# Performance work log

Measured on AMD Instinct MI355X. Metric: run time of the kernel, lower is better.

## Reference

```python
import jax, jax.numpy as jnp
import numpy as np

B, H, W, DIM, HEADS, WS, SHIFT, MLP_RATIO = 32, 56, 56, 256, 8, 7, 3, 4
N = WS * WS                      # tokens per window = 49
NW = (H // WS) * (W // WS)       # windows per image = 64
HEAD_DIM = DIM // HEADS
HIDDEN = DIM * MLP_RATIO


def _rel_index():
    # standard Swin relative position index, shape (N, N), values in [0, (2*WS-1)^2)
    coords = np.stack(np.meshgrid(np.arange(WS), np.arange(WS), indexing='ij')).reshape(2, -1)
    rel = (coords[:, :, None] - coords[:, None, :]).transpose(1, 2, 0)
    rel[:, :, 0] += WS - 1
    rel[:, :, 1] += WS - 1
    rel[:, :, 0] *= 2 * WS - 1
    return rel.sum(-1).astype(np.int32)


def _attn_mask():
    # shifted-window attention mask, shape (NW, N, N), values in {0, -100}
    img = np.zeros((H, W))
    slices = (slice(0, -WS), slice(-WS, -SHIFT), slice(-SHIFT, None))
    cnt = 0
    for hs in slices:
        for ws_ in slices:
            img[hs, ws_] = cnt
            cnt += 1
    mw = img.reshape(H // WS, WS, W // WS, WS).transpose(0, 2, 1, 3).reshape(-1, N)
    diff = mw[:, None, :] - mw[:, :, None]
    return np.where(diff != 0, -100.0, 0.0).astype(np.float32)


def setup_inputs() -> dict:
    key = jax.random.key(0)
    ks = jax.random.split(key, 16)
    s = 0.02
    return {
        'x': jax.random.normal(ks[0], (B, H * W, DIM), jnp.float32),
        'norm1_w': jnp.ones((DIM,), jnp.float32),
        'norm1_b': jnp.zeros((DIM,), jnp.float32),
        'qkv_w': jax.random.normal(ks[1], (3 * DIM, DIM), jnp.float32) * s,
        'qkv_b': jnp.zeros((3 * DIM,), jnp.float32),
        'rpb_table': jax.random.normal(ks[2], ((2 * WS - 1) ** 2, HEADS), jnp.float32) * s,
        'proj_w': jax.random.normal(ks[3], (DIM, DIM), jnp.float32) * s,
        'proj_b': jnp.zeros((DIM,), jnp.float32),
        'norm2_w': jnp.ones((DIM,), jnp.float32),
        'norm2_b': jnp.zeros((DIM,), jnp.float32),
        'fc1_w': jax.random.normal(ks[4], (HIDDEN, DIM), jnp.float32) * s,
        'fc1_b': jnp.zeros((HIDDEN,), jnp.float32),
        'fc2_w': jax.random.normal(ks[5], (DIM, HIDDEN), jnp.float32) * s,
        'fc2_b': jnp.zeros((DIM,), jnp.float32),
        'rel_idx': jnp.asarray(_rel_index()),
        'attn_mask': jnp.asarray(_attn_mask()),
    }


def _ln(t, w, b):
    mu = t.mean(-1, keepdims=True)
    var = ((t - mu) ** 2).mean(-1, keepdims=True)
    return (t - mu) * jax.lax.rsqrt(var + 1e-5) * w + b


def reference(x, norm1_w, norm1_b, qkv_w, qkv_b, rpb_table, proj_w, proj_b,
              norm2_w, norm2_b, fc1_w, fc1_b, fc2_w, fc2_b, rel_idx, attn_mask):
    Bz = x.shape[0]
    shortcut = x
    h = _ln(x, norm1_w, norm1_b).reshape(Bz, H, W, DIM)
    h = jnp.roll(h, (-SHIFT, -SHIFT), axis=(1, 2))                      # cyclic shift
    # window partition -> (Bz*NW, N, C)
    h = h.reshape(Bz, H // WS, WS, W // WS, WS, DIM).transpose(0, 1, 3, 2, 4, 5).reshape(-1, N, DIM)
    qkv = (h @ qkv_w.T + qkv_b).reshape(-1, N, 3, HEADS, HEAD_DIM).transpose(2, 0, 3, 1, 4)
    q, k, v = qkv[0], qkv[1], qkv[2]                                    # (Bz*NW, heads, N, d)
    scale = HEAD_DIM ** -0.5
    attn = jnp.einsum('whnd,whmd->whnm', q * scale, k)
    bias = rpb_table[rel_idx].transpose(2, 0, 1)                        # (heads, N, N)
    attn = attn + bias[None]
    attn = attn.reshape(Bz, NW, HEADS, N, N) + attn_mask[None, :, None]  # shift mask
    attn = jax.nn.softmax(attn.reshape(-1, HEADS, N, N), axis=-1)
    out = jnp.einsum('whnm,whmd->whnd', attn, v).transpose(0, 2, 1, 3).reshape(-1, N, DIM)
    out = out @ proj_w.T + proj_b
    # window reverse + un-shift
    out = out.reshape(Bz, H // WS, W // WS, WS, WS, DIM).transpose(0, 1, 3, 2, 4, 5).reshape(Bz, H, W, DIM)
    out = jnp.roll(out, (SHIFT, SHIFT), axis=(1, 2)).reshape(Bz, H * W, DIM)
    x = shortcut + out
    # residual MLP (pre-LN), exact GELU as in nn.GELU default
    h2 = _ln(x, norm2_w, norm2_b)
    h2 = jax.nn.gelu(h2 @ fc1_w.T + fc1_b, approximate=False)
    return x + (h2 @ fc2_w.T + fc2_b)
```

## Files before the change

kernel.cpp:

```cpp
#include <hip/hip_runtime.h>

typedef unsigned short ushort_t;
typedef __attribute__((ext_vector_type(8))) __bf16 bf16x8;
typedef __attribute__((ext_vector_type(4))) float floatx4;

#define TOKS 100352

__device__ __forceinline__ ushort_t f2bf(float f) {
    union { float f; unsigned u; } a; a.f = f;
    unsigned r = a.u + 0x7fffu + ((a.u >> 16) & 1u);
    return (ushort_t)(r >> 16);
}

__device__ __forceinline__ void async16(const void* g, void* l) {
    __builtin_amdgcn_global_load_lds(
        (const __attribute__((address_space(1))) unsigned int*)g,
        (__attribute__((address_space(3))) unsigned int*)l,
        16, 0, 0);
}

__device__ __forceinline__ int win_to_orig(int t) {
    int b = t / 3136, rr = t - b * 3136;
    int w_ = rr / 49, pos = rr - w_ * 49;
    int wi = w_ >> 3, wj = w_ & 7;
    int ti = pos / 7, tj = pos - ti * 7;
    int h = wi * 7 + ti + 3; if (h >= 56) h -= 56;
    int w = wj * 7 + tj + 3; if (w >= 56) w -= 56;
    return b * 3136 + h * 56 + w;
}

__global__ void convert_kernel(const float* __restrict__ qkv_w, const float* __restrict__ proj_w,
                               const float* __restrict__ fc1_w, const float* __restrict__ fc2_w,
                               const float* __restrict__ rpb, const int* __restrict__ rel_idx,
                               ushort_t* __restrict__ wq, ushort_t* __restrict__ wp,
                               ushort_t* __restrict__ w1, ushort_t* __restrict__ w2,
                               float* __restrict__ bias_h) {
    int i = blockIdx.x * 256 + threadIdx.x;
    if (i < 196608) wq[i] = f2bf(qkv_w[i]);
    if (i < 65536)  wp[i] = f2bf(proj_w[i]);
    if (i < 262144) { w1[i] = f2bf(fc1_w[i]); w2[i] = f2bf(fc2_w[i]); }
    if (i < 19208) {
        int h = i / 2401, ij = i - h * 2401;
        bias_h[i] = rpb[rel_idx[ij] * 8 + h];
    }
}

__global__ __launch_bounds__(256) void ln_kernel(const float* __restrict__ xin,
                                                 const float* __restrict__ gw,
                                                 const float* __restrict__ gb,
                                                 ushort_t* __restrict__ outb) {
    const int wid = threadIdx.x >> 6, lane = threadIdx.x & 63;
    const int t_out = blockIdx.x * 4 + wid;
    const int t_in = win_to_orig(t_out);
    const float4* src = (const float4*)(xin + (long)t_in * 256);
    float4 v = src[lane];
    float s  = v.x + v.y + v.z + v.w;
    float s2 = v.x*v.x + v.y*v.y + v.z*v.z + v.w*v.w;
    #pragma unroll
    for (int d = 32; d >= 1; d >>= 1) { s += __shfl_xor(s, d, 64); s2 += __shfl_xor(s2, d, 64); }
    float mu  = s * 0.00390625f;
    float var = s2 * 0.00390625f - mu * mu;
    float ry  = rsqrtf(var + 1e-5f);
    float4 w4 = ((const float4*)gw)[lane], b4 = ((const float4*)gb)[lane];
    unsigned long long p =
          (unsigned long long)f2bf((v.x - mu) * ry * w4.x + b4.x)
        | ((unsigned long long)f2bf((v.y - mu) * ry * w4.y + b4.y) << 16)
        | ((unsigned long long)f2bf((v.z - mu) * ry * w4.z + b4.z) << 32)
        | ((unsigned long long)f2bf((v.w - mu) * ry * w4.w + b4.w) << 48);
    ((unsigned long long*)(outb + (long)t_out * 256))[lane] = p;
}

template <int MODE, int N_LD, int KD>
__global__ __launch_bounds__(256, 2) void gemm_kernel(const ushort_t* __restrict__ A,
                                                      const ushort_t* __restrict__ Bw,
                                                      const float* __restrict__ bias,
                                                      void* __restrict__ outp,
                                                      const ushort_t* __restrict__ x1w,
                                                      int rowOff) {
    __shared__ __align__(16) ushort_t As[128 * 32];
    __shared__ __align__(16) ushort_t Bs[128 * 32];
    const int tid = threadIdx.x;
    const int lane = tid & 63;
    const int wid = tid >> 6;
    const int wm = wid & 1, wn = wid >> 1;
    const int l15 = lane & 15, quad = lane >> 4;
    const long tileM = (long)blockIdx.y * 128;
    const long tileN = (long)blockIdx.x * 128;

    floatx4 acc[4][4];
    #pragma unroll
    for (int i = 0; i < 4; i++)
        #pragma unroll
        for (int j = 0; j < 4; j++) acc[i][j] = {0.f, 0.f, 0.f, 0.f};

    const int o1 = tid * 16;
    const int r1 = o1 >> 6, c1 = (o1 & 63) >> 1;
    const ushort_t* Ar1 = A + (tileM + r1) * KD + c1;
    const ushort_t* Ar2 = A + (tileM + r1 + 64) * KD + c1;
    const ushort_t* Br1 = Bw + (tileN + r1) * KD + c1;
    const ushort_t* Br2 = Bw + (tileN + r1 + 64) * KD + c1;
    ushort_t* Ad1 = &As[o1 >> 1];
    ushort_t* Ad2 = &As[(o1 >> 1) + 2048];
    ushort_t* Bd1 = &Bs[o1 >> 1];
    ushort_t* Bd2 = &Bs[(o1 >> 1) + 2048];

    for (int k0 = 0; k0 < KD; k0 += 32) {
        async16(Ar1 + k0, Ad1);
        async16(Ar2 + k0, Ad2);
        async16(Br1 + k0, Bd1);
        async16(Br2 + k0, Bd2);
        __syncthreads();
        bf16x8 af[4], bfr[4];
        #pragma unroll
        for (int mi = 0; mi < 4; mi++)
            af[mi] = *(const bf16x8*)&As[(wm * 64 + mi * 16 + l15) * 32 + quad * 8];
        #pragma unroll
        for (int nj = 0; nj < 4; nj++)
            bfr[nj] = *(const bf16x8*)&Bs[(wn * 64 + nj * 16 + l15) * 32 + quad * 8];
        #pragma unroll
        for (int mi = 0; mi < 4; mi++)
            #pragma unroll
            for (int nj = 0; nj < 4; nj++)
                acc[mi][nj] = __builtin_amdgcn_mfma_f32_16x16x32_bf16(af[mi], bfr[nj], acc[mi][nj], 0, 0, 0);
        __syncthreads();
    }

    #pragma unroll
    for (int mi = 0; mi < 4; mi++)
      #pragma unroll
      for (int nj = 0; nj < 4; nj++)
        #pragma unroll
        for (int r = 0; r < 4; r++) {
            long row = tileM + wm * 64 + mi * 16 + quad * 4 + r;
            long col = tileN + wn * 64 + nj * 16 + l15;
            float v = acc[mi][nj][r] + bias[col];
            if (MODE == 0) {
                ((ushort_t*)outp)[row * N_LD + col] = f2bf(v);
            } else if (MODE == 2) {
                float g = 0.5f * v * (1.f + erff(v * 0.70710678118654752f));
                ((ushort_t*)outp)[row * N_LD + col] = f2bf(g);
            } else {
                union { ushort_t u[2]; unsigned v32; float f; } cvt;
                cvt.u[0] = 0; cvt.u[1] = x1w[row * 256 + col];
                float res = cvt.f;
                int orig = win_to_orig((int)row + rowOff);
                ((float*)outp)[(long)orig * 256 + col] = v + res;
            }
        }
}

__global__ __launch_bounds__(256, 2) void proj_ln_kernel(
        const ushort_t* __restrict__ A, const ushort_t* __restrict__ Bw,
        const float* __restrict__ pb, const float* __restrict__ x_res,
        const float* __restrict__ n2w, const float* __restrict__ n2b,
        ushort_t* __restrict__ x1w, ushort_t* __restrict__ h2out) {
    __shared__ __align__(16) ushort_t As[64 * 32];
    __shared__ __align__(16) ushort_t Bs[256 * 32];
    __shared__ float red_s[4][64];
    __shared__ float red_q[4][64];
    const int tid = threadIdx.x, lane = tid & 63, wid = tid >> 6;
    const int l15 = lane & 15, quad = lane >> 4;
    const long tileM = (long)blockIdx.x * 64;

    floatx4 acc[4][4];
    #pragma unroll
    for (int i = 0; i < 4; i++)
        #pragma unroll
        for (int j = 0; j < 4; j++) acc[i][j] = {0.f, 0.f, 0.f, 0.f};

    const int oA = tid * 16;
    const int rA = oA >> 6, cA = (oA & 63) >> 1;
    const ushort_t* Ap = A + (tileM + rA) * 256 + cA;
    ushort_t* Ad = &As[oA >> 1];

    for (int k0 = 0; k0 < 256; k0 += 32) {
        async16(Ap + k0, Ad);
        #pragma unroll
        for (int ch = 0; ch < 4; ch++) {
            int o = ch * 4096 + oA;
            async16(Bw + (o >> 6) * 256 + ((o & 63) >> 1) + k0, &Bs[o >> 1]);
        }
        __syncthreads();
        bf16x8 af[4], bfr[4];
        #pragma unroll
        for (int mi = 0; mi < 4; mi++)
            af[mi] = *(const bf16x8*)&As[(mi * 16 + l15) * 32 + quad * 8];
        #pragma unroll
        for (int nj = 0; nj < 4; nj++)
            bfr[nj] = *(const bf16x8*)&Bs[(wid * 64 + nj * 16 + l15) * 32 + quad * 8];
        #pragma unroll
        for (int mi = 0; mi < 4; mi++)
            #pragma unroll
            for (int nj = 0; nj < 4; nj++)
                acc[mi][nj] = __builtin_amdgcn_mfma_f32_16x16x32_bf16(af[mi], bfr[nj], acc[mi][nj], 0, 0, 0);
        __syncthreads();
    }

    #pragma unroll
    for (int mi = 0; mi < 4; mi++)
      #pragma unroll
      for (int r = 0; r < 4; r++) {
        int iloc = mi * 16 + quad * 4 + r;
        int orig = win_to_orig((int)tileM + iloc);
        float s = 0.f, q = 0.f;
        #pragma unroll
        for (int nj = 0; nj < 4; nj++) {
            int col = wid * 64 + nj * 16 + l15;
            float v = acc[mi][nj][r] + pb[col] + x_res[(long)orig * 256 + col];
            x1w[(tileM + iloc) * 256 + col] = f2bf(v);
            acc[mi][nj][r] = v;
            s += v; q += v * v;
        }
        #pragma unroll
        for (int d = 1; d < 16; d <<= 1) { s += __shfl_xor(s, d, 64); q += __shfl_xor(q, d, 64); }
        if (l15 == 0) { red_s[wid][iloc] = s; red_q[wid][iloc] = q; }
      }
    __syncthreads();
    #pragma unroll
    for (int mi = 0; mi < 4; mi++)
      #pragma unroll
      for (int r = 0; r < 4; r++) {
        int iloc = mi * 16 + quad * 4 + r;
        float s = red_s[0][iloc] + red_s[1][iloc] + red_s[2][iloc] + red_s[3][iloc];
        float q = red_q[0][iloc] + red_q[1][iloc] + red_q[2][iloc] + red_q[3][iloc];
        float mu = s * 0.00390625f;
        float var = q * 0.00390625f - mu * mu;
        float rstd = rsqrtf(var + 1e-5f);
        #pragma unroll
        for (int nj = 0; nj < 4; nj++) {
            int col = wid * 64 + nj * 16 + l15;
            float v = acc[mi][nj][r];
            h2out[(tileM + iloc) * 256 + col] = f2bf((v - mu) * rstd * n2w[col] + n2b[col]);
        }
      }
}

__global__ __launch_bounds__(128) void attn_kernel(const ushort_t* __restrict__ qkv,
                                                   const float* __restrict__ bias_h,
                                                   const float* __restrict__ mask,
                                                   ushort_t* __restrict__ attnout) {
    __shared__ __align__(16) ushort_t lds[2 * 6912];
    const int tid = threadIdx.x, lane = tid & 63, wid = tid >> 6;
    ushort_t* Pl = &lds[wid * 6912];
    ushort_t* Vt = Pl + 64 * 72;
    const int whid = blockIdx.x * 2 + wid;
    const int win = whid >> 3, head = whid & 7;
    const int l15 = lane & 15, quad = lane >> 4;
    const long base = (long)win * 49 * 768;
    const float* bh = bias_h + head * 2401;
    const float* mk = mask + (win & 63) * 2401;

    bf16x8 qf[4], kf[4];
    #pragma unroll
    for (int t4 = 0; t4 < 4; t4++) {
        int tok = t4 * 16 + l15; if (tok > 48) tok = 48;
        const ushort_t* p = qkv + base + (long)tok * 768 + head * 32 + quad * 8;
        qf[t4] = *(const bf16x8*)p;
        kf[t4] = *(const bf16x8*)(p + 256);
    }

    floatx4 S[4][4];
    #pragma unroll
    for (int mi = 0; mi < 4; mi++)
        #pragma unroll
        for (int nj = 0; nj < 4; nj++) {
            floatx4 z = {0.f, 0.f, 0.f, 0.f};
            S[mi][nj] = __builtin_amdgcn_mfma_f32_16x16x32_bf16(qf[mi], kf[nj], z, 0, 0, 0);
        }

    {
        int j = lane;
        int jc = j < 49 ? j : 48;
        const uint4* vsrc = (const uint4*)(qkv + base + (long)jc * 768 + 512 + head * 32);
        uint4 vz; vz.x = vz.y = vz.z = vz.w = 0u;
        #pragma unroll
        for (int q4 = 0; q4 < 4; q4++) {
            uint4 vv = (j < 49) ? vsrc[q4] : vz;
            int db = q4 * 8;
            Vt[(db+0)*72 + j] = (ushort_t)vv.x;  Vt[(db+1)*72 + j] = (ushort_t)(vv.x >> 16);
            Vt[(db+2)*72 + j] = (ushort_t)vv.y;  Vt[(db+3)*72 + j] = (ushort_t)(vv.y >> 16);
            Vt[(db+4)*72 + j] = (ushort_t)vv.z;  Vt[(db+5)*72 + j] = (ushort_t)(vv.z >> 16);
            Vt[(db+6)*72 + j] = (ushort_t)vv.w;  Vt[(db+7)*72 + j] = (ushort_t)(vv.w >> 16);
        }
    }

    const float scale = 0.17677669529663687f;
    #pragma unroll
    for (int mi = 0; mi < 4; mi++)
      #pragma unroll
      for (int nj = 0; nj < 4; nj++)
        #pragma unroll
        for (int r = 0; r < 4; r++) {
            int i = mi * 16 + quad * 4 + r;
            int j = nj * 16 + l15;
            float s = -1e30f;
            if (i < 49 && j < 49) {
                int ij = i * 49 + j;
                s = S[mi][nj][r] * scale + bh[ij] + mk[ij];
            }
            S[mi][nj][r] = s;
        }

    float rinv[4][4];
    #pragma unroll
    for (int mi = 0; mi < 4; mi++)
      #pragma unroll
      for (int r = 0; r < 4; r++) {
          float m = fmaxf(fmaxf(S[mi][0][r], S[mi][1][r]), fmaxf(S[mi][2][r], S[mi][3][r]));
          #pragma unroll
          for (int d = 1; d < 16; d <<= 1) m = fmaxf(m, __shfl_xor(m, d, 64));
          float e[4], sum = 0.f;
          #pragma unroll
          for (int nj = 0; nj < 4; nj++) { e[nj] = __expf(S[mi][nj][r] - m); sum += e[nj]; }
          #pragma unroll
          for (int d = 1; d < 16; d <<= 1) sum += __shfl_xor(sum, d, 64);
          rinv[mi][r] = 1.f / sum;
          int i = mi * 16 + quad * 4 + r;
          #pragma unroll
          for (int nj = 0; nj < 4; nj++) Pl[i * 72 + (nj * 16 + l15)] = f2bf(e[nj]);
      }

    __syncthreads();

    floatx4 O[4][2];
    #pragma unroll
    for (int mi = 0; mi < 4; mi++) { O[mi][0] = {0.f,0.f,0.f,0.f}; O[mi][1] = {0.f,0.f,0.f,0.f}; }
    #pragma unroll
    for (int kc = 0; kc < 2; kc++) {
        bf16x8 pf[4], vf[2];
        #pragma unroll
        for (int mi = 0; mi < 4; mi++)
            pf[mi] = *(const bf16x8*)&Pl[(mi * 16 + l15) * 72 + kc * 32 + quad * 8];
        #pragma unroll
        for (int n2 = 0; n2 < 2; n2++)
            vf[n2] = *(const bf16x8*)&Vt[(n2 * 16 + l15) * 72 + kc * 32 + quad * 8];
        #pragma unroll
        for (int mi = 0; mi < 4; mi++)
            #pragma unroll
            for (int n2 = 0; n2 < 2; n2++)
                O[mi][n2] = __builtin_amdgcn_mfma_f32_16x16x32_bf16(pf[mi], vf[n2], O[mi][n2], 0, 0, 0);
    }

    #pragma unroll
    for (int mi = 0; mi < 4; mi++)
      #pragma unroll
      for (int n2 = 0; n2 < 2; n2++)
        #pragma unroll
        for (int r = 0; r < 4; r++) {
            int i = mi * 16 + quad * 4 + r;
            if (i < 49) {
                long orow = ((long)win * 49 + i) * 256 + head * 32 + n2 * 16 + l15;
                attnout[orow] = f2bf(O[mi][n2][r] * rinv[mi][r]);
            }
        }
}

extern "C" void kernel_launch(void* const* d_in, const int* in_sizes, int n_in,
                              void* d_out, int out_size, void* d_ws, size_t ws_size,
                              hipStream_t stream) {
    const float* x      = (const float*)d_in[0];
    const float* n1w    = (const float*)d_in[1];
    const float* n1b    = (const float*)d_in[2];
    const float* qkv_w  = (const float*)d_in[3];
    const float* qkv_b  = (const float*)d_in[4];
    const float* rpb    = (const float*)d_in[5];
    const float* proj_w = (const float*)d_in[6];
    const float* proj_b = (const float*)d_in[7];
    const float* n2w    = (const float*)d_in[8];
    const float* n2b    = (const float*)d_in[9];
    const float* fc1_w  = (const float*)d_in[10];
    const float* fc1_b  = (const float*)d_in[11];
    const float* fc2_w  = (const float*)d_in[12];
    const float* fc2_b  = (const float*)d_in[13];
    const int*   rel_idx= (const int*)d_in[14];
    const float* amask  = (const float*)d_in[15];

    char* ws = (char*)d_ws;
    ushort_t* wq   = (ushort_t*)(ws + 0);
    ushort_t* wp   = (ushort_t*)(ws + 393216);
    ushort_t* w1   = (ushort_t*)(ws + 524288);
    ushort_t* w2   = (ushort_t*)(ws + 1048576);
    float*    bh   = (float*)   (ws + 1572864);
    ushort_t* hwin = (ushort_t*)(ws + 1649728);
    ushort_t* qkvb = (ushort_t*)(ws + 53029952);
    ushort_t* h2   = (ushort_t*)(ws + 104410176);
    ushort_t* x1w  = (ushort_t*)(ws + 155790400);
    ushort_t* h3   = hwin;

    convert_kernel<<<1024, 256, 0, stream>>>(qkv_w, proj_w, fc1_w, fc2_w, rpb, rel_idx,
                                             wq, wp, w1, w2, bh);
    ln_kernel<<<TOKS / 4, 256, 0, stream>>>(x, n1w, n1b, hwin);
    gemm_kernel<0, 768, 256><<<dim3(6, 784), 256, 0, stream>>>(hwin, wq, qkv_b, qkvb, nullptr, 0);
    attn_kernel<<<8192, 128, 0, stream>>>(qkvb, bh, amask, hwin);
    proj_ln_kernel<<<1568, 256, 0, stream>>>(hwin, wp, proj_b, x, n2w, n2b, x1w, h2);
    for (int c = 0; c < 2; c++) {
        gemm_kernel<2, 1024, 256><<<dim3(8, 392), 256, 0, stream>>>(
            h2 + (long)c * 50176 * 256, w1, fc1_b, h3, nullptr, 0);
        gemm_kernel<4, 256, 1024><<<dim3(2, 392), 256, 0, stream>>>(
            h3, w2, fc2_b, (float*)d_out, x1w + (long)c * 50176 * 256, c * 50176);
    }
    (void)in_sizes; (void)n_in; (void)out_size; (void)ws_size;
}
```

Before: 750.7 us.

## Premerge bias+mask into bf16 table, swizzle GEMM tiles, widen attention blocks

Precomputes a per-window-per-head bf16 table that combines the relative position bias and the shift mask, stored temporarily in the output buffer. The attention kernel then does one load per score instead of two fp32 loads. GEMM launches switch to a 1D grid that groups tiles so 8 row tiles sweep the column tiles together, aiming for better L2 reuse. Attention blocks now run 4 waves with smaller LDS per wave. The risks are bf16 rounding of bias+mask and relying on the output buffer being overwritten later.

New measurement: 658.7 us. -12.3%, faster.

```diff
diff --git a/kernel.cpp b/kernel.cpp
--- a/kernel.cpp
+++ b/kernel.cpp
@@ -10,6 +10,9 @@
     union { float f; unsigned u; } a; a.f = f;
     unsigned r = a.u + 0x7fffu + ((a.u >> 16) & 1u);
     return (ushort_t)(r >> 16);
+}
+__device__ __forceinline__ float bf2f(ushort_t u) {
+    union { unsigned v; float f; } a; a.v = ((unsigned)u) << 16; return a.f;
 }
 
 __device__ __forceinline__ void async16(const void* g, void* l) {
@@ -32,16 +35,18 @@
 __global__ void convert_kernel(const float* __restrict__ qkv_w, const float* __restrict__ proj_w,
                                const float* __restrict__ fc1_w, const float* __restrict__ fc2_w,
                                const float* __restrict__ rpb, const int* __restrict__ rel_idx,
+                               const float* __restrict__ amask,
                                ushort_t* __restrict__ wq, ushort_t* __restrict__ wp,
                                ushort_t* __restrict__ w1, ushort_t* __restrict__ w2,
-                               float* __restrict__ bias_h) {
+                               ushort_t* __restrict__ bm) {
     int i = blockIdx.x * 256 + threadIdx.x;
     if (i < 196608) wq[i] = f2bf(qkv_w[i]);
     if (i < 65536)  wp[i] = f2bf(proj_w[i]);
     if (i < 262144) { w1[i] = f2bf(fc1_w[i]); w2[i] = f2bf(fc2_w[i]); }
-    if (i < 19208) {
-        int h = i / 2401, ij = i - h * 2401;
-        bias_h[i] = rpb[rel_idx[ij] * 8 + h];
+    if (i < 1229312) {
+        int wh = i / 2401, ij = i - wh * 2401;
+        int head = wh & 7, wimg = wh >> 3;
+        bm[i] = f2bf(rpb[rel_idx[ij] * 8 + head] + amask[wimg * 2401 + ij]);
     }
 }
 
@@ -70,7 +75,7 @@
     ((unsigned long long*)(outb + (long)t_out * 256))[lane] = p;
 }
 
-template <int MODE, int N_LD, int KD>
+template <int MODE, int N_LD, int KD, int CT>
 __global__ __launch_bounds__(256, 2) void gemm_kernel(const ushort_t* __restrict__ A,
                                                       const ushort_t* __restrict__ Bw,
                                                       const float* __restrict__ bias,
@@ -84,14 +89,16 @@
     const int wid = tid >> 6;
     const int wm = wid & 1, wn = wid >> 1;
     const int l15 = lane & 15, quad = lane >> 4;
-    const long tileM = (long)blockIdx.y * 128;
-    const long tileN = (long)blockIdx.x * 128;
+    const int v = blockIdx.x;
+    const int j = v >> 3;
+    const long tileM = (long)((j / CT) * 8 + (v & 7)) * 128;
+    const long tileN = (long)(j % CT) * 128;
 
     floatx4 acc[4][4];
     #pragma unroll
     for (int i = 0; i < 4; i++)
         #pragma unroll
-        for (int j = 0; j < 4; j++) acc[i][j] = {0.f, 0.f, 0.f, 0.f};
+        for (int jj = 0; jj < 4; jj++) acc[i][jj] = {0.f, 0.f, 0.f, 0.f};
 
     const int o1 = tid * 16;
     const int r1 = o1 >> 6, c1 = (o1 & 63) >> 1;
@@ -133,18 +140,16 @@
         for (int r = 0; r < 4; r++) {
             long row = tileM + wm * 64 + mi * 16 + quad * 4 + r;
             long col = tileN + wn * 64 + nj * 16 + l15;
-            float v = acc[mi][nj][r] + bias[col];
+            float val = acc[mi][nj][r] + bias[col];
             if (MODE == 0) {
-                ((ushort_t*)outp)[row * N_LD + col] = f2bf(v);
+                ((ushort_t*)outp)[row * N_LD + col] = f2bf(val);
             } else if (MODE == 2) {
-                float g = 0.5f * v * (1.f + erff(v * 0.70710678118654752f));
+                float g = 0.5f * val * (1.f + erff(val * 0.70710678118654752f));
                 ((ushort_t*)outp)[row * N_LD + col] = f2bf(g);
             } else {
-                union { ushort_t u[2]; unsigned v32; float f; } cvt;
-                cvt.u[0] = 0; cvt.u[1] = x1w[row * 256 + col];
-                float res = cvt.f;
+                float res = bf2f(x1w[row * 256 + col]);
                 int orig = win_to_orig((int)row + rowOff);
-                ((float*)outp)[(long)orig * 256 + col] = v + res;
+                ((float*)outp)[(long)orig * 256 + col] = val + res;
             }
         }
 }
@@ -206,10 +211,10 @@
         #pragma unroll
         for (int nj = 0; nj < 4; nj++) {
             int col = wid * 64 + nj * 16 + l15;
-            float v = acc[mi][nj][r] + pb[col] + x_res[(long)orig * 256 + col];
-            x1w[(tileM + iloc) * 256 + col] = f2bf(v);
-            acc[mi][nj][r] = v;
-            s += v; q += v * v;
+            float val = acc[mi][nj][r] + pb[col] + x_res[(long)orig * 256 + col];
+            x1w[(tileM + iloc) * 256 + col] = f2bf(val);
+            acc[mi][nj][r] = val;
+            s += val; q += val * val;
         }
         #pragma unroll
         for (int d = 1; d < 16; d <<= 1) { s += __shfl_xor(s, d, 64); q += __shfl_xor(q, d, 64); }
@@ -229,26 +234,24 @@
         #pragma unroll
         for (int nj = 0; nj < 4; nj++) {
             int col = wid * 64 + nj * 16 + l15;
-            float v = acc[mi][nj][r];
-            h2out[(tileM + iloc) * 256 + col] = f2bf((v - mu) * rstd * n2w[col] + n2b[col]);
+            float val = acc[mi][nj][r];
+            h2out[(tileM + iloc) * 256 + col] = f2bf((val - mu) * rstd * n2w[col] + n2b[col]);
         }
       }
 }
 
-__global__ __launch_bounds__(128) void attn_kernel(const ushort_t* __restrict__ qkv,
-                                                   const float* __restrict__ bias_h,
-                                                   const float* __restrict__ mask,
+__global__ __launch_bounds__(256) void attn_kernel(const ushort_t* __restrict__ qkv,
+                                                   const ushort_t* __restrict__ bm,
                                                    ushort_t* __restrict__ attnout) {
-    __shared__ __align__(16) ushort_t lds[2 * 6912];
+    __shared__ __align__(16) ushort_t lds[4 * 5832];
     const int tid = threadIdx.x, lane = tid & 63, wid = tid >> 6;
-    ushort_t* Pl = &lds[wid * 6912];
-    ushort_t* Vt = Pl + 64 * 72;
-    const int whid = blockIdx.x * 2 + wid;
+    ushort_t* Pl = &lds[wid * 5832];
+    ushort_t* Vt = Pl + 49 * 72;
+    const int whid = blockIdx.x * 4 + wid;
     const int win = whid >> 3, head = whid & 7;
     const int l15 = lane & 15, quad = lane >> 4;
     const long base = (long)win * 49 * 768;
-    const float* bh = bias_h + head * 2401;
-    const float* mk = mask + (win & 63) * 2401;
+    const ushort_t* bmw = bm + (long)((win & 63) * 8 + head) * 2401;
 
     bf16x8 qf[4], kf[4];
     #pragma unroll
@@ -269,18 +272,18 @@
         }
 
     {
-        int j = lane;
-        int jc = j < 49 ? j : 48;
+        int jl = lane;
+        int jc = jl < 49 ? jl : 48;
         const uint4* vsrc = (const uint4*)(qkv + base + (long)jc * 768 + 512 + head * 32);
         uint4 vz; vz.x = vz.y = vz.z = vz.w = 0u;
         #pragma unroll
         for (int q4 = 0; q4 < 4; q4++) {
-            uint4 vv = (j < 49) ? vsrc[q4] : vz;
+            uint4 vv = (jl < 49) ? vsrc[q4] : vz;
             int db = q4 * 8;
-            Vt[(db+0)*72 + j] = (ushort_t)vv.x;  Vt[(db+1)*72 + j] = (ushort_t)(vv.x >> 16);
-            Vt[(db+2)*72 + j] = (ushort_t)vv.y;  Vt[(db+3)*72 + j] = (ushort_t)(vv.y >> 16);
-            Vt[(db+4)*72 + j] = (ushort_t)vv.z;  Vt[(db+5)*72 + j] = (ushort_t)(vv.z >> 16);
-            Vt[(db+6)*72 + j] = (ushort_t)vv.w;  Vt[(db+7)*72 + j] = (ushort_t)(vv.w >> 16);
+            Vt[(db+0)*72 + jl] = (ushort_t)vv.x;  Vt[(db+1)*72 + jl] = (ushort_t)(vv.x >> 16);
+            Vt[(db+2)*72 + jl] = (ushort_t)vv.y;  Vt[(db+3)*72 + jl] = (ushort_t)(vv.y >> 16);
+            Vt[(db+4)*72 + jl] = (ushort_t)vv.z;  Vt[(db+5)*72 + jl] = (ushort_t)(vv.z >> 16);
+            Vt[(db+6)*72 + jl] = (ushort_t)vv.w;  Vt[(db+7)*72 + jl] = (ushort_t)(vv.w >> 16);
         }
     }
 
@@ -292,12 +295,9 @@
         #pragma unroll
         for (int r = 0; r < 4; r++) {
             int i = mi * 16 + quad * 4 + r;
-            int j = nj * 16 + l15;
+            int jj = nj * 16 + l15;
             float s = -1e30f;
-            if (i < 49 && j < 49) {
-                int ij = i * 49 + j;
-                s = S[mi][nj][r] * scale + bh[ij] + mk[ij];
-            }
+            if (i < 49 && jj < 49) s = S[mi][nj][r] * scale + bf2f(bmw[i * 49 + jj]);
             S[mi][nj][r] = s;
         }
 
@@ -316,8 +316,10 @@
           for (int d = 1; d < 16; d <<= 1) sum += __shfl_xor(sum, d, 64);
           rinv[mi][r] = 1.f / sum;
           int i = mi * 16 + quad * 4 + r;
-          #pragma unroll
-          for (int nj = 0; nj < 4; nj++) Pl[i * 72 + (nj * 16 + l15)] = f2bf(e[nj]);
+          if (i < 49) {
+              #pragma unroll
+              for (int nj = 0; nj < 4; nj++) Pl[i * 72 + (nj * 16 + l15)] = f2bf(e[nj]);
+          }
       }
 
     __syncthreads();
@@ -329,8 +331,10 @@
     for (int kc = 0; kc < 2; kc++) {
         bf16x8 pf[4], vf[2];
         #pragma unroll
-        for (int mi = 0; mi < 4; mi++)
-            pf[mi] = *(const bf16x8*)&Pl[(mi * 16 + l15) * 72 + kc * 32 + quad * 8];
+        for (int mi = 0; mi < 4; mi++) {
+            int pr = mi * 16 + l15; if (pr > 48) pr = 48;
+            pf[mi] = *(const bf16x8*)&Pl[pr * 72 + kc * 32 + quad * 8];
+        }
         #pragma unroll
         for (int n2 = 0; n2 < 2; n2++)
             vf[n2] = *(const bf16x8*)&Vt[(n2 * 16 + l15) * 72 + kc * 32 + quad * 8];
@@ -380,23 +384,23 @@
     ushort_t* wp   = (ushort_t*)(ws + 393216);
     ushort_t* w1   = (ushort_t*)(ws + 524288);
     ushort_t* w2   = (ushort_t*)(ws + 1048576);
-    float*    bh   = (float*)   (ws + 1572864);
-    ushort_t* hwin = (ushort_t*)(ws + 1649728);
-    ushort_t* qkvb = (ushort_t*)(ws + 53029952);
-    ushort_t* h2   = (ushort_t*)(ws + 104410176);
-    ushort_t* x1w  = (ushort_t*)(ws + 155790400);
+    ushort_t* hwin = (ushort_t*)(ws + 1572864);
+    ushort_t* qkvb = (ushort_t*)(ws + 52953088);
+    ushort_t* h2   = (ushort_t*)(ws + 104333312);
+    ushort_t* x1w  = (ushort_t*)(ws + 155713536);
     ushort_t* h3   = hwin;
-
-    convert_kernel<<<1024, 256, 0, stream>>>(qkv_w, proj_w, fc1_w, fc2_w, rpb, rel_idx,
-                                             wq, wp, w1, w2, bh);
+    ushort_t* bm = (ushort_t*)d_out;
+
+    convert_kernel<<<4803, 256, 0, stream>>>(qkv_w, proj_w, fc1_w, fc2_w, rpb, rel_idx,
+                                             amask, wq, wp, w1, w2, bm);
     ln_kernel<<<TOKS / 4, 256, 0, stream>>>(x, n1w, n1b, hwin);
-    gemm_kernel<0, 768, 256><<<dim3(6, 784), 256, 0, stream>>>(hwin, wq, qkv_b, qkvb, nullptr, 0);
-    attn_kernel<<<8192, 128, 0, stream>>>(qkvb, bh, amask, hwin);
+    gemm_kernel<0, 768, 256, 6><<<4704, 256, 0, stream>>>(hwin, wq, qkv_b, qkvb, nullptr, 0);
+    attn_kernel<<<4096, 256, 0, stream>>>(qkvb, bm, hwin);
     proj_ln_kernel<<<1568, 256, 0, stream>>>(hwin, wp, proj_b, x, n2w, n2b, x1w, h2);
     for (int c = 0; c < 2; c++) {
-        gemm_kernel<2, 1024, 256><<<dim3(8, 392), 256, 0, stream>>>(
+        gemm_kernel<2, 1024, 256, 8><<<3136, 256, 0, stream>>>(
             h2 + (long)c * 50176 * 256, w1, fc1_b, h3, nullptr, 0);
-        gemm_kernel<4, 256, 1024><<<dim3(2, 392), 256, 0, stream>>>(
+        gemm_kernel<4, 256, 1024, 2><<<784, 256, 0, stream>>>(
             h3, w2, fc2_b, (float*)d_out, x1w + (long)c * 50176 * 256, c * 50176);
     }
     (void)in_sizes; (void)n_in; (void)out_size; (void)ws_size;
```
